# Optimization experiments

Hardware: AMD Instinct MI355X
Metric: run time of the kernel (lower is better)

## Reference

```python
import jax, jax.numpy as jnp
from jax import lax
import numpy as np


def _conv(x, w, b, pad):
    y = lax.conv_general_dilated(x, w, (1, 1), [(pad, pad), (pad, pad)],
                                 dimension_numbers=('NCHW', 'OIHW', 'NCHW'))
    return y + b[None, :, None, None]


def _bn(x, g, b, eps=1e-5):
    # training-mode batchnorm (batch statistics, biased variance) like torch default
    m = jnp.mean(x, (0, 2, 3), keepdims=True)
    v = jnp.mean((x - m) ** 2, (0, 2, 3), keepdims=True)
    return g[None, :, None, None] * (x - m) * lax.rsqrt(v + eps) + b[None, :, None, None]


def _maxpool2(x):
    return lax.reduce_window(x, -jnp.inf, lax.max, (1, 1, 2, 2), (1, 1, 2, 2), 'VALID')


def _power_features(x):
    # vectorized version of the per-image FFT + radial-bin histogram mean
    B, _, H, W = x.shape
    cy, cx = H // 2, W // 2
    yy, xx = jnp.meshgrid(jnp.arange(H), jnp.arange(W), indexing='ij')
    r = jnp.sqrt((xx - cx).astype(jnp.float32) ** 2 + (yy - cy).astype(jnp.float32) ** 2)
    max_r = min(H, W) // 2
    NB = 32
    r_bins = jnp.linspace(0.0, float(max_r), NB + 1)
    # bin j covers [r_bins[j], r_bins[j+1]) exactly as the torch mask
    idx = jnp.searchsorted(r_bins, r.ravel(), side='right') - 1
    valid = (idx >= 0) & (idx < NB)
    seg = jnp.where(valid, idx, NB)  # dump out-of-range into bin NB
    counts = jax.ops.segment_sum(valid.astype(jnp.float32), seg, NB + 1)[:NB]
    ps = jnp.abs(jnp.fft.fft2(x[:, 0])) ** 2  # [B,H,W]
    psf = ps.reshape(B, -1) * valid.astype(ps.dtype)[None, :]
    sums = jax.vmap(lambda p: jax.ops.segment_sum(p, seg, NB + 1))(psf)[:, :NB]
    radial = jnp.where(counts > 0, sums / jnp.maximum(counts, 1.0), 0.0)
    return jnp.log(radial + 1e-10)  # [B,32]


def reference(x, cw1, cb1, g1, bb1, cw2, cb2, g2, bb2, cw3, cb3, g3, bb3,
              cw4, cb4, g4, bb4, pcw, pcb, pg, pbb,
              pw1, pb1, pw2, pb2, pw3, pb3,
              fw1, fb1, fw2, fb2, fw3, fb3, fw4, fb4):
    h = jax.nn.relu(_bn(_conv(x, cw1, cb1, 2), g1, bb1)); h = _maxpool2(h)
    h = jax.nn.relu(_bn(_conv(h, cw2, cb2, 2), g2, bb2)); h = _maxpool2(h)
    h = jax.nn.relu(_bn(_conv(h, cw3, cb3, 1), g3, bb3)); h = _maxpool2(h)
    h = jax.nn.relu(_bn(_conv(h, cw4, cb4, 1), g4, bb4))        # [B,256,32,32]
    p = jax.nn.relu(_bn(_conv(h, pcw, pcb, 1), pg, pbb))        # [B,128,32,32]
    # adaptive avg pool (4,4): exact 8x8 windows, stride 8
    p = lax.reduce_window(p, 0.0, lax.add, (1, 1, 8, 8), (1, 1, 8, 8), 'VALID') / 64.0
    flat = p.reshape(p.shape[0], -1)  # [B,2048]
    pf = _power_features(x)           # [B,32]
    pf = jax.nn.relu(pf @ pw1.T + pb1)
    pf = jax.nn.relu(pf @ pw2.T + pb2)
    pf = jax.nn.relu(pf @ pw3.T + pb3)  # [B,64]
    c = jnp.concatenate([flat, pf], axis=1)  # [B,2112]
    c = jax.nn.relu(c @ fw1.T + fb1)
    c = jax.nn.relu(c @ fw2.T + fb2)
    c = jax.nn.relu(c @ fw3.T + fb3)
    return c @ fw4.T + fb4  # [B,2]


def setup_inputs() -> dict:
    key = jax.random.key(0)
    ki = iter(jax.random.split(key, 40))

    def W(shape):
        fan_in = int(np.prod(shape[1:]))
        return jax.random.normal(next(ki), shape, jnp.float32) / np.sqrt(fan_in)

    d = {'x': jax.random.normal(next(ki), (16, 1, 256, 256), jnp.float32)}
    convs = [('cw1', 'cb1', 'g1', 'bb1', (32, 1, 5, 5)),
             ('cw2', 'cb2', 'g2', 'bb2', (64, 32, 5, 5)),
             ('cw3', 'cb3', 'g3', 'bb3', (128, 64, 3, 3)),
             ('cw4', 'cb4', 'g4', 'bb4', (256, 128, 3, 3)),
             ('pcw', 'pcb', 'pg', 'pbb', (128, 256, 3, 3))]
    for wn, bn, gn, ben, s in convs:
        d[wn] = W(s); d[bn] = jnp.zeros(s[0], jnp.float32)
        d[gn] = jnp.ones(s[0], jnp.float32); d[ben] = jnp.zeros(s[0], jnp.float32)
    lins = [('pw1', 'pb1', (256, 32)), ('pw2', 'pb2', (128, 256)), ('pw3', 'pb3', (64, 128)),
            ('fw1', 'fb1', (512, 2112)), ('fw2', 'fb2', (256, 512)),
            ('fw3', 'fb3', (128, 256)), ('fw4', 'fb4', (2, 128))]
    for wn, bn, s in lins:
        d[wn] = W(s); d[bn] = jnp.zeros(s[0], jnp.float32)
    return d
```

## Files before the change

kernel.cpp:

```cpp
#include <hip/hip_runtime.h>
#include <math.h>


#define PI2F 6.283185307179586f

typedef _Float16 half8 __attribute__((ext_vector_type(8)));
typedef _Float16 half4v __attribute__((ext_vector_type(4)));
typedef float f32x4 __attribute__((ext_vector_type(4)));


__device__ __forceinline__ int bitrev8(int x) {
  x = ((x & 0x0F) << 4) | ((x >> 4) & 0x0F);
  x = ((x & 0x33) << 2) | ((x >> 2) & 0x33);
  x = ((x & 0x55) << 1) | ((x >> 1) & 0x55);
  return x;
}

__global__ __launch_bounds__(64)
void fft_rows(const float* __restrict__ x, float2* __restrict__ out) {
  __shared__ float2 s[256];
  __shared__ float2 tw[128];
  int blk = blockIdx.x;
  const float* rowp = x + (size_t)blk * 256;
  int t = threadIdx.x;
  for (int i = t; i < 128; i += 64) {
    float sn, cs;
    sincosf(-(PI2F / 256.f) * (float)i, &sn, &cs);
    tw[i] = make_float2(cs, sn);
  }
  #pragma unroll
  for (int e = 0; e < 4; ++e) {
    int i = t + (e << 6);
    s[bitrev8(i)] = make_float2(rowp[i], 0.f);
  }
  __syncthreads();
  #pragma unroll
  for (int st = 1; st <= 8; ++st) {
    int half = 1 << (st - 1);
    #pragma unroll
    for (int j = 0; j < 2; ++j) {
      int bf = t + (j << 6);
      int pos = bf & (half - 1);
      int grp = bf >> (st - 1);
      int i0 = (grp << st) | pos;
      int i1 = i0 + half;
      int k = pos << (8 - st);
      float cs = tw[k].x, sn = tw[k].y;
      float2 a = s[i0], b = s[i1];
      float tr = cs * b.x - sn * b.y;
      float ti = cs * b.y + sn * b.x;
      s[i0] = make_float2(a.x + tr, a.y + ti);
      s[i1] = make_float2(a.x - tr, a.y - ti);
    }
    __syncthreads();
  }
  float2* op = out + (size_t)blk * 256;
  #pragma unroll
  for (int e = 0; e < 4; ++e) { int i = t + (e << 6); op[i] = s[i]; }
}

__device__ __forceinline__ int radial_bin(int r2) {
  int j = (int)(sqrtf((float)r2) * 0.25f);
  while ((j + 1) * (j + 1) * 16 <= r2) ++j;
  while (j > 0 && j * j * 16 > r2) --j;
  return j;
}

__global__ __launch_bounds__(256)
void fft_cols_radial_v2(const float2* __restrict__ f, float* __restrict__ radial) {
  __shared__ float2 s[8][258];
  __shared__ float2 tw[128];
  __shared__ float bins[8][32];
  int b = blockIdx.x >> 5;
  int col0 = (blockIdx.x & 31) * 8;
  int t = threadIdx.x;
  for (int i = t; i < 128; i += 256) {
    float sn, cs;
    sincosf(-(PI2F / 256.f) * (float)i, &sn, &cs);
    tw[i] = make_float2(cs, sn);
  }
  ((float*)bins)[t] = 0.f;
  for (int idx = t; idx < 2048; idx += 256) {
    int row = idx >> 3, c = idx & 7;
    s[c][bitrev8(row)] = f[(size_t)b * 65536 + row * 256 + col0 + c];
  }
  __syncthreads();
  int c = t >> 5, l = t & 31;
  float2* sc = &s[c][0];
  #pragma unroll
  for (int st = 1; st <= 8; ++st) {
    int half = 1 << (st - 1);
    #pragma unroll
    for (int j = 0; j < 4; ++j) {
      int bf = l + (j << 5);
      int pos = bf & (half - 1);
      int grp = bf >> (st - 1);
      int i0 = (grp << st) | pos;
      int i1 = i0 + half;
      int k = pos << (8 - st);
      float cs = tw[k].x, sn = tw[k].y;
      float2 a = sc[i0], bb = sc[i1];
      float tr = cs * bb.x - sn * bb.y;
      float ti = cs * bb.y + sn * bb.x;
      sc[i0] = make_float2(a.x + tr, a.y + ti);
      sc[i1] = make_float2(a.x - tr, a.y - ti);
    }
    __syncthreads();
  }
  int dx = col0 + c - 128;
  #pragma unroll
  for (int e = 0; e < 8; ++e) {
    int i = l * 8 + e;
    float2 v = sc[i];
    float ps = v.x * v.x + v.y * v.y;
    int dy = i - 128;
    int r2 = dx * dx + dy * dy;
    if (r2 < 16384) atomicAdd(&bins[c][radial_bin(r2)], ps);
  }
  __syncthreads();
  if (t < 32) {
    float s0 = bins[0][t] + bins[1][t] + bins[2][t] + bins[3][t] +
               bins[4][t] + bins[5][t] + bins[6][t] + bins[7][t];
    atomicAdd(&radial[b * 32 + t], s0);
  }
}

__device__ __forceinline__ int isqrt_(int v) {
  int r = (int)sqrtf((float)v);
  while (r * r > v) --r;
  while ((r + 1) * (r + 1) <= v) ++r;
  return r;
}

__global__ __launch_bounds__(256)
void radial_finalize_v3(const float* __restrict__ radial, float* __restrict__ pf0) {
  __shared__ int red[4];
  __shared__ int cnt_s;
  int j = blockIdx.x, t = threadIdx.x;
  int dy = t - 128;
  int lo = 16 * j * j, hi = 16 * (j + 1) * (j + 1);
  int d2 = dy * dy;
  int cnt = 0;
  int tHi = hi - 1 - d2;
  if (tHi >= 0) {
    int rHi = isqrt_(tHi);
    int nHi = min(rHi, 127) + min(rHi, 128) + 1;
    int nLo = 0;
    int tLo = lo - 1 - d2;
    if (tLo >= 0) { int rLo = isqrt_(tLo); nLo = min(rLo, 127) + min(rLo, 128) + 1; }
    cnt = nHi - nLo;
  }
  #pragma unroll
  for (int off = 32; off > 0; off >>= 1) cnt += __shfl_down(cnt, off);
  if ((t & 63) == 0) red[t >> 6] = cnt;
  __syncthreads();
  if (t == 0) cnt_s = red[0] + red[1] + red[2] + red[3];
  __syncthreads();
  if (t < 16) {
    float cf = (float)cnt_s;
    float sum = radial[t * 32 + j];
    float val = cf > 0.f ? sum / fmaxf(cf, 1.f) : 0.f;
    pf0[t * 32 + j] = logf(val + 1e-10f);
  }
}


__global__ __launch_bounds__(256)
void wtrans_all(const float* __restrict__ cw2, const float* __restrict__ cw3,
                const float* __restrict__ cw4, const float* __restrict__ pcw,
                _Float16* __restrict__ wb2, _Float16* __restrict__ wb3,
                _Float16* __restrict__ wb4, _Float16* __restrict__ wbp) {
  int blk = blockIdx.x;
  const float* src; _Float16* dst; int COUT, CIN, KK, i;
  if (blk < 200)       { src = cw2; dst = wb2; COUT = 64;  CIN = 32;  KK = 25; i = blk * 256; }
  else if (blk < 488)  { src = cw3; dst = wb3; COUT = 128; CIN = 64;  KK = 9;  i = (blk - 200) * 256; }
  else if (blk < 1640) { src = cw4; dst = wb4; COUT = 256; CIN = 128; KK = 9;  i = (blk - 488) * 256; }
  else                 { src = pcw; dst = wbp; COUT = 128; CIN = 256; KK = 9;  i = (blk - 1640) * 256; }
  i += threadIdx.x;
  if (i >= COUT * CIN * KK) return;
  int ci = i % CIN;
  int r = i / CIN;
  int co = r % COUT;
  int tap = r / COUT;
  dst[i] = (_Float16)src[((size_t)co * CIN + ci) * KK + tap];
}


__device__ __forceinline__ void load16(float* d, const float* p) {
  f32x4 v0 = *(const f32x4*)(p);
  f32x4 v1 = *(const f32x4*)(p + 4);
  f32x4 v2 = *(const f32x4*)(p + 8);
  f32x4 v3 = *(const f32x4*)(p + 12);
  #pragma unroll
  for (int e = 0; e < 4; ++e) { d[e] = v0[e]; d[4+e] = v1[e]; d[8+e] = v2[e]; d[12+e] = v3[e]; }
}

__global__ __launch_bounds__(256)
void conv1_stats_v3(const float* __restrict__ x, const float* __restrict__ w,
                    float* __restrict__ stats) {
  __shared__ float lds[12 * 264];
  __shared__ float r1[4][32], r2[4][32];
  int t = threadIdx.x;
  int y0 = blockIdx.x * 8, n = blockIdx.y;
  const float* xp = x + (size_t)n * 65536;
  for (int i = t; i < 12 * 264; i += 256) {
    int r = i / 264, cc = i % 264;
    int gy = y0 + r - 2, gx = cc - 4;
    lds[i] = (gy >= 0 && gy < 256 && gx >= 0 && gx < 256) ? xp[gy * 256 + gx] : 0.f;
  }
  __syncthreads();
  int c = t & 31, xg = t >> 5;
  float wreg[25];
  #pragma unroll
  for (int k = 0; k < 25; ++k) wreg[k] = w[c * 25 + k];
  float s1 = 0.f, s2 = 0.f;
  for (int strip = 0; strip < 4; ++strip) {
    int px0 = xg * 8 + strip * 64;
    float f[5][16];
    #pragma unroll
    for (int rr = 0; rr < 4; ++rr) load16(f[rr], &lds[rr * 264 + px0]);
    #pragma unroll
    for (int r = 0; r < 8; ++r) {
      load16(f[(r + 4) % 5], &lds[(r + 4) * 264 + px0]);
      f32x4 A = {0.f, 0.f, 0.f, 0.f}, B = {0.f, 0.f, 0.f, 0.f};
      #pragma unroll
      for (int ky = 0; ky < 5; ++ky) {
        const float* fr = f[(r + ky) % 5];
        #pragma unroll
        for (int kx = 0; kx < 5; ++kx) {
          float wv = wreg[ky * 5 + kx];
          f32x4 ia = {fr[2 + kx], fr[3 + kx], fr[4 + kx], fr[5 + kx]};
          f32x4 ib = {fr[6 + kx], fr[7 + kx], fr[8 + kx], fr[9 + kx]};
          A += wv * ia; B += wv * ib;
        }
      }
      s1 += A[0] + A[1] + A[2] + A[3] + B[0] + B[1] + B[2] + B[3];
      s2 += A[0]*A[0] + A[1]*A[1] + A[2]*A[2] + A[3]*A[3]
          + B[0]*B[0] + B[1]*B[1] + B[2]*B[2] + B[3]*B[3];
    }
  }
  s1 += __shfl_down(s1, 32);
  s2 += __shfl_down(s2, 32);
  if ((t & 63) < 32) { r1[t >> 6][t & 31] = s1; r2[t >> 6][t & 31] = s2; }
  __syncthreads();
  if (t < 32) {
    atomicAdd(&stats[t],      r1[0][t] + r1[1][t] + r1[2][t] + r1[3][t]);
    atomicAdd(&stats[32 + t], r2[0][t] + r2[1][t] + r2[2][t] + r2[3][t]);
  }
}

__global__ __launch_bounds__(256)
void conv1_apply_v3(const float* __restrict__ x, const float* __restrict__ w,
                    const float* __restrict__ stats, const float* __restrict__ g,
                    const float* __restrict__ bb, _Float16* __restrict__ pool1) {
  __shared__ float lds[6 * 264];
  int t = threadIdx.x;
  int py = blockIdx.x, n = blockIdx.y;
  const float* xp = x + (size_t)n * 65536;
  for (int i = t; i < 6 * 264; i += 256) {
    int r = i / 264, cc = i % 264;
    int gy = 2 * py + r - 2, gx = cc - 4;
    lds[i] = (gy >= 0 && gy < 256 && gx >= 0 && gx < 256) ? xp[gy * 256 + gx] : 0.f;
  }
  __syncthreads();
  int c = t & 31, xg = t >> 5;
  float wreg[25];
  #pragma unroll
  for (int k = 0; k < 25; ++k) wreg[k] = w[c * 25 + k];
  float mean = stats[c] * (1.f / 1048576.f);
  float var  = stats[32 + c] * (1.f / 1048576.f) - mean * mean;
  float sc = g[c] / sqrtf(var + 1e-5f);
  float sh = bb[c] - mean * sc;
  for (int iter = 0; iter < 4; ++iter) {
    int p0 = xg * 4 + iter * 32;
    float f[6][16];
    #pragma unroll
    for (int rr = 0; rr < 6; ++rr) load16(f[rr], &lds[rr * 264 + 2 * p0]);
    f32x4 acc[2][2];
    #pragma unroll
    for (int sy = 0; sy < 2; ++sy)
      #pragma unroll
      for (int h = 0; h < 2; ++h) acc[sy][h] = (f32x4){0.f, 0.f, 0.f, 0.f};
    #pragma unroll
    for (int sy = 0; sy < 2; ++sy)
      #pragma unroll
      for (int ky = 0; ky < 5; ++ky) {
        const float* fr = f[sy + ky];
        #pragma unroll
        for (int kx = 0; kx < 5; ++kx) {
          float wv = wreg[ky * 5 + kx];
          f32x4 ia = {fr[2 + kx], fr[3 + kx], fr[4 + kx], fr[5 + kx]};
          f32x4 ib = {fr[6 + kx], fr[7 + kx], fr[8 + kx], fr[9 + kx]};
          acc[sy][0] += wv * ia; acc[sy][1] += wv * ib;
        }
      }
    #pragma unroll
    for (int pp = 0; pp < 4; ++pp) {
      float v00 = acc[0][(2*pp) >> 2][(2*pp) & 3];
      float v01 = acc[0][(2*pp+1) >> 2][(2*pp+1) & 3];
      float v10 = acc[1][(2*pp) >> 2][(2*pp) & 3];
      float v11 = acc[1][(2*pp+1) >> 2][(2*pp+1) & 3];
      float m = fmaxf(fmaxf(v00, v01), fmaxf(v10, v11));
      pool1[(((size_t)n * 128 + py) * 128 + p0 + pp) * 32 + c] =
          (_Float16)fmaxf(m * sc + sh, 0.f);
    }
  }
}


template <int CIN, int COUT, int H, int W, int K, int TH, int TW, int COT,
          int PT, int SLAB>
__global__ __launch_bounds__(256)
void conv_mfma2(const _Float16* __restrict__ in, const _Float16* __restrict__ wb,
                _Float16* __restrict__ out, float* __restrict__ stats) {
  constexpr int P = K / 2, R = TH + 2 * P, XW = TW + 2 * P, PIX = R * XW;
  constexpr int TAPS = K * K, CSP = SLAB + 8;
  constexpr int NCC = SLAB / 32, NPH = CIN / SLAB, SUBS = SLAB / 8;
  static_assert(TH * TW == 32 * PT, "pos tile mismatch");
  __shared__ _Float16 lds[PIX * CSP];
  __shared__ float sst[2][32 * COT];
  int t = threadIdx.x;
  int lane = t & 63, wv = t >> 6;
  int lane15 = lane & 15, quad = lane >> 4;
  constexpr int WT = W / TW;
  int x0 = (blockIdx.x % WT) * TW, y0 = (blockIdx.x / WT) * TH;
  int coB = blockIdx.y * (32 * COT);
  int nb = blockIdx.z;
  int co_off = (wv & 1) * (16 * COT);
  int pos_off = (wv >> 1) * (16 * PT);

  for (int i = t; i < 64 * COT; i += 256) ((float*)sst)[i] = 0.f;

  f32x4 acc[COT][PT];
  #pragma unroll
  for (int ct = 0; ct < COT; ++ct)
    #pragma unroll
    for (int pt = 0; pt < PT; ++pt)
      #pragma unroll
      for (int e = 0; e < 4; ++e) acc[ct][pt][e] = 0.f;

  int bbase[PT];
  #pragma unroll
  for (int pt = 0; pt < PT; ++pt) {
    int np = pos_off + pt * 16 + lane15;
    int ly = np / TW, lx = np % TW;
    bbase[pt] = (ly * XW + lx) * CSP + quad * 8;
  }
  const _Float16* aptr[COT];
  #pragma unroll
  for (int ct = 0; ct < COT; ++ct)
    aptr[ct] = wb + (size_t)(coB + co_off + ct * 16 + lane15) * CIN + quad * 8;

  const _Float16* inb = in + (size_t)nb * H * W * CIN;

  #pragma unroll
  for (int ph = 0; ph < NPH; ++ph) {
    constexpr int ITEMS = PIX * SUBS;
    for (int i = t; i < ITEMS; i += 256) {
      int sub = i % SUBS, pix = i / SUBS;
      int r = pix / XW, xx = pix % XW;
      int gy = y0 + r - P, gx = x0 + xx - P;
      half8 v;
      #pragma unroll
      for (int j = 0; j < 8; ++j) v[j] = (_Float16)0.f;
      if (gy >= 0 && gy < H && gx >= 0 && gx < W)
        v = *(const half8*)(inb + ((size_t)gy * W + gx) * CIN + ph * SLAB + sub * 8);
      *(half8*)(&lds[pix * CSP + sub * 8]) = v;
    }
    __syncthreads();
    #pragma unroll
    for (int cc = 0; cc < NCC; ++cc) {
      #pragma unroll
      for (int tap = 0; tap < TAPS; ++tap) {
        int ky = tap / K, kx = tap % K;
        half8 a[COT], b[PT];
        #pragma unroll
        for (int ct = 0; ct < COT; ++ct)
          a[ct] = *(const half8*)(aptr[ct] + (size_t)tap * COUT * CIN +
                                  ph * SLAB + cc * 32);
        #pragma unroll
        for (int pt = 0; pt < PT; ++pt)
          b[pt] = *(const half8*)(&lds[bbase[pt] + (ky * XW + kx) * CSP + cc * 32]);
        #pragma unroll
        for (int ct = 0; ct < COT; ++ct)
          #pragma unroll
          for (int pt = 0; pt < PT; ++pt)
            acc[ct][pt] = __builtin_amdgcn_mfma_f32_16x16x32_f16(
                a[ct], b[pt], acc[ct][pt], 0, 0, 0);
      }
    }
    if (ph + 1 < NPH) __syncthreads();
  }

  #pragma unroll
  for (int ct = 0; ct < COT; ++ct)
    #pragma unroll
    for (int pt = 0; pt < PT; ++pt) {
      int co = coB + co_off + ct * 16 + quad * 4;
      int np = pos_off + pt * 16 + lane15;
      int y = y0 + np / TW, x = x0 + np % TW;
      _Float16* op = out + (((size_t)nb * H + y) * W + x) * COUT + co;
      half4v h;
      #pragma unroll
      for (int e = 0; e < 4; ++e) h[e] = (_Float16)acc[ct][pt][e];
      *(half4v*)op = h;
    }
  #pragma unroll
  for (int ct = 0; ct < COT; ++ct)
    #pragma unroll
    for (int e = 0; e < 4; ++e) {
      float sv = 0.f, sq = 0.f;
      #pragma unroll
      for (int pt = 0; pt < PT; ++pt) {
        float v = acc[ct][pt][e];
        sv += v; sq += v * v;
      }
      sv += __shfl_xor(sv, 1); sq += __shfl_xor(sq, 1);
      sv += __shfl_xor(sv, 2); sq += __shfl_xor(sq, 2);
      sv += __shfl_xor(sv, 4); sq += __shfl_xor(sq, 4);
      sv += __shfl_xor(sv, 8); sq += __shfl_xor(sq, 8);
      if (lane15 == 0) {
        int cl = co_off + ct * 16 + quad * 4 + e;
        atomicAdd(&sst[0][cl], sv);
        atomicAdd(&sst[1][cl], sq);
      }
    }
  __syncthreads();
  float* st = stats + (blockIdx.x & 7) * 2 * COUT;
  for (int i = t; i < 32 * COT; i += 256) {
    atomicAdd(&st[coB + i], sst[0][i]);
    atomicAdd(&st[COUT + coB + i], sst[1][i]);
  }
}


__device__ __forceinline__ void bn_coeff(const float* stats, int C, int c,
                                         float invN, const float* g,
                                         const float* bb, float* sc, float* sh) {
  float s1 = 0.f, s2 = 0.f;
  #pragma unroll
  for (int s = 0; s < 8; ++s) {
    s1 += stats[s * 2 * C + c];
    s2 += stats[s * 2 * C + C + c];
  }
  float mean = s1 * invN;
  float var  = s2 * invN - mean * mean;
  float k = g[c] / sqrtf(var + 1e-5f);
  *sc = k; *sh = bb[c] - mean * k;
}

__global__ __launch_bounds__(256)
void bn_pool_nhwc(const _Float16* __restrict__ x, const float* __restrict__ stats,
                  const float* __restrict__ g, const float* __restrict__ bb,
                  _Float16* __restrict__ out, int C, int H, int W, float invN) {
  __shared__ float scs[256], shs[256];
  int t = threadIdx.x;
  int py = blockIdx.x, n = blockIdx.y;
  for (int c = t; c < C; c += 256) bn_coeff(stats, C, c, invN, g, bb, &scs[c], &shs[c]);
  __syncthreads();
  int W2 = W >> 1;
  int tot = W2 * C;
  for (int i = t; i < tot; i += 256) {
    int c = i % C, px = i / C;
    const _Float16* p0 = x + (((size_t)n * H + 2 * py) * W + 2 * px) * C + c;
    float sc = scs[c], sh = shs[c];
    float a = fmaxf((float)p0[0] * sc + sh, 0.f);
    float b = fmaxf((float)p0[C] * sc + sh, 0.f);
    float d = fmaxf((float)p0[(size_t)W * C] * sc + sh, 0.f);
    float e = fmaxf((float)p0[(size_t)W * C + C] * sc + sh, 0.f);
    out[(((size_t)n * (H / 2) + py) * W2 + px) * C + c] =
        (_Float16)fmaxf(fmaxf(a, b), fmaxf(d, e));
  }
}

__global__ __launch_bounds__(256)
void bn_relu_h16(const _Float16* __restrict__ x, const float* __restrict__ stats,
                 const float* __restrict__ g, const float* __restrict__ bb,
                 _Float16* __restrict__ out, int C, int HW, float invN) {
  __shared__ float scs[256], shs[256];
  int t = threadIdx.x;
  int n = blockIdx.y;
  for (int c = t; c < C; c += 256) bn_coeff(stats, C, c, invN, g, bb, &scs[c], &shs[c]);
  __syncthreads();
  int total = HW * C;
  int chunk = total / gridDim.x;
  int base = blockIdx.x * chunk;
  const _Float16* xp = x + (size_t)n * total;
  _Float16* op = out + (size_t)n * total;
  for (int i = base + t; i < base + chunk; i += 256) {
    int c = i % C;
    op[i] = (_Float16)fmaxf((float)xp[i] * scs[c] + shs[c], 0.f);
  }
}

__global__ __launch_bounds__(256)
void bn_avgpool_concat(const _Float16* __restrict__ x, const float* __restrict__ stats,
                       const float* __restrict__ g, const float* __restrict__ bb,
                       float* __restrict__ concat, float invN) {
  __shared__ float scs[128], shs[128];
  int t = threadIdx.x;
  int n = blockIdx.x;
  for (int c = t; c < 128; c += 256) bn_coeff(stats, 128, c, invN, g, bb, &scs[c], &shs[c]);
  __syncthreads();
  for (int i = t; i < 2048; i += 256) {
    int c = i & 127, opix = i >> 7;
    int py = opix >> 2, px = opix & 3;
    float sc = scs[c], sh = shs[c];
    float s = 0.f;
    for (int yy = 0; yy < 8; ++yy)
      for (int xx = 0; xx < 8; ++xx)
        s += fmaxf((float)x[(((size_t)n * 32 + py * 8 + yy) * 32 + px * 8 + xx) * 128 + c] * sc + sh, 0.f);
    concat[(size_t)n * 2112 + c * 16 + opix] = s * (1.f / 64.f);
  }
}


__global__ __launch_bounds__(64)
void linear_k(const float* __restrict__ in, const float* __restrict__ w,
              const float* __restrict__ bias, float* __restrict__ out,
              int I, int in_stride, int out_stride, int relu) {
  int o = blockIdx.x, b = blockIdx.y;
  int lane = threadIdx.x;
  const float* ip = in + (size_t)b * in_stride;
  const float* wp = w + (size_t)o * I;
  float acc = 0.f;
  for (int i = lane; i < I; i += 64) acc += ip[i] * wp[i];
  #pragma unroll
  for (int off = 32; off > 0; off >>= 1) acc += __shfl_down(acc, off);
  if (lane == 0) {
    float v = acc + bias[o];
    if (relu) v = fmaxf(v, 0.f);
    out[(size_t)b * out_stride + o] = v;
  }
}

__global__ __launch_bounds__(256)
void pf_mlp(const float* __restrict__ pf0,
            const float* __restrict__ pw1, const float* __restrict__ pb1,
            const float* __restrict__ pw2, const float* __restrict__ pb2,
            const float* __restrict__ pw3, const float* __restrict__ pb3,
            float* __restrict__ concat) {
  __shared__ float a0[32], a1[256], a2[128];
  int b = blockIdx.x, t = threadIdx.x;
  if (t < 32) a0[t] = pf0[b * 32 + t];
  __syncthreads();
  {
    float s = pb1[t];
    for (int i = 0; i < 32; ++i) s += pw1[t * 32 + i] * a0[i];
    a1[t] = fmaxf(s, 0.f);
  }
  __syncthreads();
  if (t < 128) {
    float s = pb2[t];
    for (int i = 0; i < 256; ++i) s += pw2[t * 256 + i] * a1[i];
    a2[t] = fmaxf(s, 0.f);
  }
  __syncthreads();
  if (t < 64) {
    float s = pb3[t];
    for (int i = 0; i < 128; ++i) s += pw3[t * 128 + i] * a2[i];
    concat[(size_t)b * 2112 + 2048 + t] = fmaxf(s, 0.f);
  }
}

__global__ __launch_bounds__(256)
void fc_tail(const float* __restrict__ fc1o,
             const float* __restrict__ fw2, const float* __restrict__ fb2,
             const float* __restrict__ fw3, const float* __restrict__ fb3,
             const float* __restrict__ fw4, const float* __restrict__ fb4,
             float* __restrict__ out) {
  __shared__ float a1[512], a2[256], a3[128];
  int b = blockIdx.x, t = threadIdx.x;
  a1[t] = fc1o[b * 512 + t];
  a1[t + 256] = fc1o[b * 512 + t + 256];
  __syncthreads();
  {
    float s = fb2[t];
    for (int i = 0; i < 512; ++i) s += fw2[t * 512 + i] * a1[i];
    a2[t] = fmaxf(s, 0.f);
  }
  __syncthreads();
  if (t < 128) {
    float s = fb3[t];
    for (int i = 0; i < 256; ++i) s += fw3[t * 256 + i] * a2[i];
    a3[t] = fmaxf(s, 0.f);
  }
  __syncthreads();
  if (t < 2) {
    float s = fb4[t];
    for (int i = 0; i < 128; ++i) s += fw4[t * 128 + i] * a3[i];
    out[b * 2 + t] = s;
  }
}


extern "C" void kernel_launch(void* const* d_in, const int* in_sizes, int n_in,
                              void* d_out, int out_size, void* d_ws, size_t ws_size,
                              hipStream_t stream) {
  (void)in_sizes; (void)n_in; (void)out_size; (void)ws_size;
  const float* x   = (const float*)d_in[0];
  const float* cw1 = (const float*)d_in[1];
  const float* g1  = (const float*)d_in[3];
  const float* bb1 = (const float*)d_in[4];
  const float* cw2 = (const float*)d_in[5];
  const float* g2  = (const float*)d_in[7];
  const float* bb2 = (const float*)d_in[8];
  const float* cw3 = (const float*)d_in[9];
  const float* g3  = (const float*)d_in[11];
  const float* bb3 = (const float*)d_in[12];
  const float* cw4 = (const float*)d_in[13];
  const float* g4  = (const float*)d_in[15];
  const float* bb4 = (const float*)d_in[16];
  const float* pcw = (const float*)d_in[17];
  const float* pg  = (const float*)d_in[19];
  const float* pbb = (const float*)d_in[20];
  const float* pw1 = (const float*)d_in[21];
  const float* pb1 = (const float*)d_in[22];
  const float* pw2 = (const float*)d_in[23];
  const float* pb2 = (const float*)d_in[24];
  const float* pw3 = (const float*)d_in[25];
  const float* pb3 = (const float*)d_in[26];
  const float* fw1 = (const float*)d_in[27];
  const float* fb1 = (const float*)d_in[28];
  const float* fw2 = (const float*)d_in[29];
  const float* fb2 = (const float*)d_in[30];
  const float* fw3 = (const float*)d_in[31];
  const float* fb3 = (const float*)d_in[32];
  const float* fw4 = (const float*)d_in[33];
  const float* fb4 = (const float*)d_in[34];

  char* base = (char*)d_ws;
  float2*    fftbuf = (float2*)(base + 0);
  _Float16*  conv2o = (_Float16*)(base + 0);
  _Float16*  conv3o = (_Float16*)(base + 0);
  _Float16*  conv4o = (_Float16*)(base + 0);
  _Float16*  pconvo = (_Float16*)(base + 16777216);
  _Float16*  pool1  = (_Float16*)(base + 33554432);
  _Float16*  pool2  = (_Float16*)(base + 50331648);
  _Float16*  pool3  = (_Float16*)(base + 58720256);
  _Float16*  act4   = (_Float16*)(base + 62914560);
  _Float16*  wb2    = (_Float16*)(base + 71303168);
  _Float16*  wb3    = (_Float16*)(base + 71405568);
  _Float16*  wb4    = (_Float16*)(base + 71553024);
  _Float16*  wbp    = (_Float16*)(base + 72142848);
  float*     zbase  = (float*)(base + 72732672);
  float*     stats1 = zbase;
  float*     stats2 = zbase + 64;
  float*     stats3 = zbase + 1088;
  float*     stats4 = zbase + 3136;
  float*     stats5 = zbase + 7232;
  float*     radial = zbase + 9280;
  float*     pf0    = (float*)(base + 72771840);
  float*     concat = (float*)(base + 72773888);
  float*     fc1o   = (float*)(base + 72909056);

  hipMemsetAsync(zbase, 0, 9792 * sizeof(float), stream);

  wtrans_all<<<2792, 256, 0, stream>>>(cw2, cw3, cw4, pcw, wb2, wb3, wb4, wbp);

  fft_rows<<<4096, 64, 0, stream>>>(x, fftbuf);
  fft_cols_radial_v2<<<512, 256, 0, stream>>>(fftbuf, radial);
  radial_finalize_v3<<<32, 256, 0, stream>>>(radial, pf0);
  pf_mlp<<<16, 256, 0, stream>>>(pf0, pw1, pb1, pw2, pb2, pw3, pb3, concat);

  conv1_stats_v3<<<dim3(32, 16), 256, 0, stream>>>(x, cw1, stats1);
  conv1_apply_v3<<<dim3(128, 16), 256, 0, stream>>>(x, cw1, stats1, g1, bb1, pool1);

  conv_mfma2<32, 64, 128, 128, 5, 8, 16, 2, 4, 32>
      <<<dim3(128, 1, 16), 256, 0, stream>>>(pool1, wb2, conv2o, stats2);
  bn_pool_nhwc<<<dim3(64, 16), 256, 0, stream>>>(
      conv2o, stats2, g2, bb2, pool2, 64, 128, 128, 1.f / 262144.f);

  conv_mfma2<64, 128, 64, 64, 3, 8, 16, 4, 4, 64>
      <<<dim3(32, 1, 16), 256, 0, stream>>>(pool2, wb3, conv3o, stats3);
  bn_pool_nhwc<<<dim3(32, 16), 256, 0, stream>>>(
      conv3o, stats3, g3, bb3, pool3, 128, 64, 64, 1.f / 65536.f);

  conv_mfma2<128, 256, 32, 32, 3, 4, 16, 2, 2, 128>
      <<<dim3(16, 4, 16), 256, 0, stream>>>(pool3, wb4, conv4o, stats4);
  bn_relu_h16<<<dim3(8, 16), 256, 0, stream>>>(
      conv4o, stats4, g4, bb4, act4, 256, 1024, 1.f / 16384.f);

  conv_mfma2<256, 128, 32, 32, 3, 4, 16, 2, 2, 128>
      <<<dim3(16, 2, 16), 256, 0, stream>>>(act4, wbp, pconvo, stats5);
  bn_avgpool_concat<<<16, 256, 0, stream>>>(pconvo, stats5, pg, pbb, concat, 1.f / 16384.f);

  linear_k<<<dim3(512, 16), 64, 0, stream>>>(concat, fw1, fb1, fc1o, 2112, 2112, 512, 1);
  fc_tail<<<16, 256, 0, stream>>>(fc1o, fw2, fb2, fw3, fb3, fw4, fb4, (float*)d_out);
}
```

Baseline: 453.4 us.

## Fuse 2x2 max/min pooling into MFMA conv epilogue and select by BN sign

```diff
diff --git a/kernel.cpp b/kernel.cpp
--- a/kernel.cpp
+++ b/kernel.cpp
@@ -308,28 +308,32 @@
 }
 
 
-template <int CIN, int COUT, int H, int W, int K, int TH, int TW, int COT,
-          int PT, int SLAB>
-__global__ __launch_bounds__(256)
-void conv_mfma2(const _Float16* __restrict__ in, const _Float16* __restrict__ wb,
-                _Float16* __restrict__ out, float* __restrict__ stats) {
+template <int CIN, int COUT, int H, int W, int K, int TH, int TW, int CW,
+          int COT, int PT, int SLAB, int POOL>
+__global__ __launch_bounds__(256)
+void conv_mfma3(const _Float16* __restrict__ in, const _Float16* __restrict__ wb,
+                _Float16* __restrict__ out, float* __restrict__ stats,
+                size_t minoff) {
   constexpr int P = K / 2, R = TH + 2 * P, XW = TW + 2 * P, PIX = R * XW;
   constexpr int TAPS = K * K, CSP = SLAB + 8;
   constexpr int NCC = SLAB / 32, NPH = CIN / SLAB, SUBS = SLAB / 8;
-  static_assert(TH * TW == 32 * PT, "pos tile mismatch");
+  constexpr int PW = 4 / CW, COB = CW * 16 * COT;
+  static_assert(TH * TW == PW * 16 * PT, "pos tile mismatch");
+  static_assert(TW == 16, "row-per-fragment requires TW=16");
+  static_assert(!POOL || (PT % 2 == 0), "pool needs even PT");
   __shared__ _Float16 lds[PIX * CSP];
-  __shared__ float sst[2][32 * COT];
+  __shared__ float sst[2][COB];
   int t = threadIdx.x;
   int lane = t & 63, wv = t >> 6;
   int lane15 = lane & 15, quad = lane >> 4;
   constexpr int WT = W / TW;
   int x0 = (blockIdx.x % WT) * TW, y0 = (blockIdx.x / WT) * TH;
-  int coB = blockIdx.y * (32 * COT);
+  int coB = blockIdx.y * COB;
   int nb = blockIdx.z;
-  int co_off = (wv & 1) * (16 * COT);
-  int pos_off = (wv >> 1) * (16 * PT);
-
-  for (int i = t; i < 64 * COT; i += 256) ((float*)sst)[i] = 0.f;
+  int co_off = (wv % CW) * (16 * COT);
+  int rowbase = (wv / CW) * PT;
+
+  for (int i = t; i < 2 * COB; i += 256) ((float*)sst)[i] = 0.f;
 
   f32x4 acc[COT][PT];
   #pragma unroll
@@ -341,11 +345,8 @@
 
   int bbase[PT];
   #pragma unroll
-  for (int pt = 0; pt < PT; ++pt) {
-    int np = pos_off + pt * 16 + lane15;
-    int ly = np / TW, lx = np % TW;
-    bbase[pt] = (ly * XW + lx) * CSP + quad * 8;
-  }
+  for (int pt = 0; pt < PT; ++pt)
+    bbase[pt] = ((rowbase + pt) * XW + lane15) * CSP + quad * 8;
   const _Float16* aptr[COT];
   #pragma unroll
   for (int ct = 0; ct < COT; ++ct)
@@ -392,19 +393,44 @@
     if (ph + 1 < NPH) __syncthreads();
   }
 
-  #pragma unroll
-  for (int ct = 0; ct < COT; ++ct)
-    #pragma unroll
-    for (int pt = 0; pt < PT; ++pt) {
-      int co = coB + co_off + ct * 16 + quad * 4;
-      int np = pos_off + pt * 16 + lane15;
-      int y = y0 + np / TW, x = x0 + np % TW;
-      _Float16* op = out + (((size_t)nb * H + y) * W + x) * COUT + co;
-      half4v h;
-      #pragma unroll
-      for (int e = 0; e < 4; ++e) h[e] = (_Float16)acc[ct][pt][e];
-      *(half4v*)op = h;
-    }
+  if (POOL) {
+    #pragma unroll
+    for (int ct = 0; ct < COT; ++ct)
+      #pragma unroll
+      for (int pp = 0; pp < PT; pp += 2) {
+        half4v hmax, hmin;
+        #pragma unroll
+        for (int e = 0; e < 4; ++e) {
+          float vmx = fmaxf(acc[ct][pp][e], acc[ct][pp + 1][e]);
+          float vmn = fminf(acc[ct][pp][e], acc[ct][pp + 1][e]);
+          float omx = fmaxf(vmx, __shfl_xor(vmx, 1));
+          float omn = fminf(vmn, __shfl_xor(vmn, 1));
+          hmax[e] = (_Float16)omx; hmin[e] = (_Float16)omn;
+        }
+        if ((lane15 & 1) == 0) {
+          int co = coB + co_off + ct * 16 + quad * 4;
+          int prow = (y0 + rowbase + pp) >> 1;
+          int pcol = (x0 >> 1) + (lane15 >> 1);
+          size_t idx = (((size_t)nb * (H / 2) + prow) * (W / 2) + pcol) * COUT + co;
+          *(half4v*)(out + idx) = hmax;
+          *(half4v*)(out + minoff + idx) = hmin;
+        }
+      }
+  } else {
+    #pragma unroll
+    for (int ct = 0; ct < COT; ++ct)
+      #pragma unroll
+      for (int pt = 0; pt < PT; ++pt) {
+        int co = coB + co_off + ct * 16 + quad * 4;
+        int y = y0 + rowbase + pt, x = x0 + lane15;
+        _Float16* op = out + (((size_t)nb * H + y) * W + x) * COUT + co;
+        half4v h;
+        #pragma unroll
+        for (int e = 0; e < 4; ++e) h[e] = (_Float16)acc[ct][pt][e];
+        *(half4v*)op = h;
+      }
+  }
+
   #pragma unroll
   for (int ct = 0; ct < COT; ++ct)
     #pragma unroll
@@ -427,7 +453,7 @@
     }
   __syncthreads();
   float* st = stats + (blockIdx.x & 7) * 2 * COUT;
-  for (int i = t; i < 32 * COT; i += 256) {
+  for (int i = t; i < COB; i += 256) {
     atomicAdd(&st[coB + i], sst[0][i]);
     atomicAdd(&st[COUT + coB + i], sst[1][i]);
   }
@@ -450,26 +476,20 @@
 }
 
 __global__ __launch_bounds__(256)
-void bn_pool_nhwc(const _Float16* __restrict__ x, const float* __restrict__ stats,
-                  const float* __restrict__ g, const float* __restrict__ bb,
-                  _Float16* __restrict__ out, int C, int H, int W, float invN) {
+void bn_relu_sel(const _Float16* __restrict__ raw, const float* __restrict__ stats,
+                 const float* __restrict__ g, const float* __restrict__ bb,
+                 _Float16* __restrict__ out, int C, int total, float invN,
+                 size_t minoff) {
   __shared__ float scs[256], shs[256];
-  int t = threadIdx.x;
-  int py = blockIdx.x, n = blockIdx.y;
+  int t = threadIdx.x, n = blockIdx.y;
   for (int c = t; c < C; c += 256) bn_coeff(stats, C, c, invN, g, bb, &scs[c], &shs[c]);
   __syncthreads();
-  int W2 = W >> 1;
-  int tot = W2 * C;
-  for (int i = t; i < tot; i += 256) {
-    int c = i % C, px = i / C;
-    const _Float16* p0 = x + (((size_t)n * H + 2 * py) * W + 2 * px) * C + c;
-    float sc = scs[c], sh = shs[c];
-    float a = fmaxf((float)p0[0] * sc + sh, 0.f);
-    float b = fmaxf((float)p0[C] * sc + sh, 0.f);
-    float d = fmaxf((float)p0[(size_t)W * C] * sc + sh, 0.f);
-    float e = fmaxf((float)p0[(size_t)W * C + C] * sc + sh, 0.f);
-    out[(((size_t)n * (H / 2) + py) * W2 + px) * C + c] =
-        (_Float16)fmaxf(fmaxf(a, b), fmaxf(d, e));
+  for (int i = blockIdx.x * 256 + t; i < total; i += gridDim.x * 256) {
+    int c = i % C;
+    size_t idx = (size_t)n * total + i;
+    float sc = scs[c];
+    float v = sc >= 0.f ? (float)raw[idx] : (float)raw[minoff + idx];
+    out[idx] = (_Float16)fmaxf(sc * v + shs[c], 0.f);
   }
 }
 
@@ -630,29 +650,29 @@
   const float* fb4 = (const float*)d_in[34];
 
   char* base = (char*)d_ws;
-  float2*    fftbuf = (float2*)(base + 0);
-  _Float16*  conv2o = (_Float16*)(base + 0);
-  _Float16*  conv3o = (_Float16*)(base + 0);
-  _Float16*  conv4o = (_Float16*)(base + 0);
-  _Float16*  pconvo = (_Float16*)(base + 16777216);
-  _Float16*  pool1  = (_Float16*)(base + 33554432);
-  _Float16*  pool2  = (_Float16*)(base + 50331648);
-  _Float16*  pool3  = (_Float16*)(base + 58720256);
-  _Float16*  act4   = (_Float16*)(base + 62914560);
-  _Float16*  wb2    = (_Float16*)(base + 71303168);
-  _Float16*  wb3    = (_Float16*)(base + 71405568);
-  _Float16*  wb4    = (_Float16*)(base + 71553024);
-  _Float16*  wbp    = (_Float16*)(base + 72142848);
-  float*     zbase  = (float*)(base + 72732672);
-  float*     stats1 = zbase;
-  float*     stats2 = zbase + 64;
-  float*     stats3 = zbase + 1088;
-  float*     stats4 = zbase + 3136;
-  float*     stats5 = zbase + 7232;
-  float*     radial = zbase + 9280;
-  float*     pf0    = (float*)(base + 72771840);
-  float*     concat = (float*)(base + 72773888);
-  float*     fc1o   = (float*)(base + 72909056);
+  float2*    fftbuf   = (float2*)(base + 0);
+  _Float16*  pool2raw = (_Float16*)(base + 0);
+  _Float16*  pool3raw = (_Float16*)(base + 0);
+  _Float16*  conv4raw = (_Float16*)(base + 0);
+  _Float16*  pconvo   = (_Float16*)(base + 8388608);
+  _Float16*  pool1    = (_Float16*)(base + 16777216);
+  _Float16*  pool2    = (_Float16*)(base + 33554432);
+  _Float16*  pool3    = (_Float16*)(base + 41943040);
+  _Float16*  act4     = (_Float16*)(base + 46137344);
+  _Float16*  wb2      = (_Float16*)(base + 54525952);
+  _Float16*  wb3      = (_Float16*)(base + 54628352);
+  _Float16*  wb4      = (_Float16*)(base + 54775808);
+  _Float16*  wbp      = (_Float16*)(base + 55365632);
+  float*     zbase    = (float*)(base + 55955456);
+  float*     stats1   = zbase;
+  float*     stats2   = zbase + 64;
+  float*     stats3   = zbase + 1088;
+  float*     stats4   = zbase + 3136;
+  float*     stats5   = zbase + 7232;
+  float*     radial   = zbase + 9280;
+  float*     pf0      = (float*)(base + 55994624);
+  float*     concat   = (float*)(base + 55996672);
+  float*     fc1o     = (float*)(base + 56131840);
 
   hipMemsetAsync(zbase, 0, 9792 * sizeof(float), stream);
 
@@ -666,23 +686,23 @@
   conv1_stats_v3<<<dim3(32, 16), 256, 0, stream>>>(x, cw1, stats1);
   conv1_apply_v3<<<dim3(128, 16), 256, 0, stream>>>(x, cw1, stats1, g1, bb1, pool1);
 
-  conv_mfma2<32, 64, 128, 128, 5, 8, 16, 2, 4, 32>
-      <<<dim3(128, 1, 16), 256, 0, stream>>>(pool1, wb2, conv2o, stats2);
-  bn_pool_nhwc<<<dim3(64, 16), 256, 0, stream>>>(
-      conv2o, stats2, g2, bb2, pool2, 64, 128, 128, 1.f / 262144.f);
-
-  conv_mfma2<64, 128, 64, 64, 3, 8, 16, 4, 4, 64>
-      <<<dim3(32, 1, 16), 256, 0, stream>>>(pool2, wb3, conv3o, stats3);
-  bn_pool_nhwc<<<dim3(32, 16), 256, 0, stream>>>(
-      conv3o, stats3, g3, bb3, pool3, 128, 64, 64, 1.f / 65536.f);
-
-  conv_mfma2<128, 256, 32, 32, 3, 4, 16, 2, 2, 128>
-      <<<dim3(16, 4, 16), 256, 0, stream>>>(pool3, wb4, conv4o, stats4);
+  conv_mfma3<32, 64, 128, 128, 5, 16, 16, 1, 4, 4, 32, 1>
+      <<<dim3(64, 1, 16), 256, 0, stream>>>(pool1, wb2, pool2raw, stats2, 4194304);
+  bn_relu_sel<<<dim3(64, 16), 256, 0, stream>>>(
+      pool2raw, stats2, g2, bb2, pool2, 64, 262144, 1.f / 262144.f, 4194304);
+
+  conv_mfma3<64, 128, 64, 64, 3, 8, 16, 2, 4, 4, 64, 1>
+      <<<dim3(32, 1, 16), 256, 0, stream>>>(pool2, wb3, pool3raw, stats3, 2097152);
+  bn_relu_sel<<<dim3(32, 16), 256, 0, stream>>>(
+      pool3raw, stats3, g3, bb3, pool3, 128, 131072, 1.f / 65536.f, 2097152);
+
+  conv_mfma3<128, 256, 32, 32, 3, 4, 16, 2, 4, 2, 128, 0>
+      <<<dim3(16, 2, 16), 256, 0, stream>>>(pool3, wb4, conv4raw, stats4, 0);
   bn_relu_h16<<<dim3(8, 16), 256, 0, stream>>>(
-      conv4o, stats4, g4, bb4, act4, 256, 1024, 1.f / 16384.f);
-
-  conv_mfma2<256, 128, 32, 32, 3, 4, 16, 2, 2, 128>
-      <<<dim3(16, 2, 16), 256, 0, stream>>>(act4, wbp, pconvo, stats5);
+      conv4raw, stats4, g4, bb4, act4, 256, 1024, 1.f / 16384.f);
+
+  conv_mfma3<256, 128, 32, 32, 3, 4, 16, 2, 2, 2, 128, 0>
+      <<<dim3(16, 2, 16), 256, 0, stream>>>(act4, wbp, pconvo, stats5, 0);
   bn_avgpool_concat<<<16, 256, 0, stream>>>(pconvo, stats5, pg, pbb, concat, 1.f / 16384.f);
 
   linear_k<<<dim3(512, 16), 64, 0, stream>>>(concat, fw1, fb1, fc1o, 2112, 2112, 512, 1);
```

Result: slower. 466.9 us (+3.0%).
